# Kernel tuning notes

Measured on AMD Instinct MI355X. Metric: run time of the kernel, lower is better.

## Reference

```python
import jax, jax.numpy as jnp
import numpy as np
import math

B, S, D, H, L, V = 2, 2048, 1024, 16, 2, 32000
HD = D // H          # head_dim = 64
FF = 4 * D           # ffn hidden = 4096
NEG_INF = -1e9


def setup_inputs() -> dict:
    key = jax.random.key(0)
    ks = jax.random.split(key, 12)
    w = lambda k, shape: jax.random.normal(k, shape, dtype=jnp.float32) * 0.02
    return {
        "tokens": jax.random.randint(ks[0], (B, S), 0, V),
        "tok_emb": w(ks[1], (V, D)),
        "pos_emb": w(ks[2], (S, D)),
        # torch nn.Linear weights are [out, in]; stacked over layers
        "wq": w(ks[3], (L, D, D)),
        "wk": w(ks[4], (L, D, D)),
        "wv": w(ks[5], (L, D, D)),
        "wo": w(ks[6], (L, D, D)),
        "w1": w(ks[7], (L, FF, D)),
        "w2": w(ks[8], (L, D, FF)),
        "ln1_g": jnp.ones((L, D)), "ln1_b": jnp.zeros((L, D)),
        "ln2_g": jnp.ones((L, D)), "ln2_b": jnp.zeros((L, D)),
        "lnf_g": jnp.ones((D,)), "lnf_b": jnp.zeros((D,)),
        "w_out": w(ks[9], (V, D)),
    }


def _layernorm(x, g, b):
    m = jnp.mean(x, axis=-1, keepdims=True)
    v = jnp.mean(jnp.square(x - m), axis=-1, keepdims=True)
    return (x - m) * jax.lax.rsqrt(v + 1e-5) * g + b


def _transformer(tokens, tok_emb, pos_emb, wq, wk, wv, wo, w1, w2,
                 ln1_g, ln1_b, ln2_g, ln2_b, lnf_g, lnf_b, w_out):
    s = tokens.shape[1]
    # causal additive mask [1,1,S,S]
    mask = jnp.where(jnp.tril(jnp.ones((s, s), dtype=bool)), 0.0, NEG_INF)[None, None]
    h = tok_emb[tokens] + pos_emb[None, :s]
    scale = 1.0 / math.sqrt(HD)
    for l in range(L):
        # pre-norm attention
        a_in = _layernorm(h, ln1_g[l], ln1_b[l])
        q = (a_in @ wq[l].T).reshape(B, s, H, HD)
        k = (a_in @ wk[l].T).reshape(B, s, H, HD)
        v = (a_in @ wv[l].T).reshape(B, s, H, HD)
        scores = jnp.einsum('bqhd,bkhd->bhqk', q, k) * scale + mask
        attn = jax.nn.softmax(scores.astype(jnp.float32), axis=-1).astype(h.dtype)
        o = jnp.einsum('bhqk,bkhd->bqhd', attn, v).reshape(B, s, D)
        h = h + o @ wo[l].T
        # pre-norm ReLU FFN
        f_in = _layernorm(h, ln2_g[l], ln2_b[l])
        h = h + jax.nn.relu(f_in @ w1[l].T) @ w2[l].T
    h = _layernorm(h, lnf_g, lnf_b)
    return h @ w_out.T  # [B,S,V]


def reference(tokens, tok_emb, pos_emb, wq, wk, wv, wo, w1, w2,
              ln1_g, ln1_b, ln2_g, ln2_b, lnf_g, lnf_b, w_out):
    return _transformer(tokens, tok_emb, pos_emb, wq, wk, wv, wo, w1, w2,
                        ln1_g, ln1_b, ln2_g, ln2_b, lnf_g, lnf_b, w_out)
```

## Files before the change

### kernel.cpp

```cpp
#include <hip/hip_runtime.h>

#define Bv 2
#define Sv 2048
#define Dv 1024
#define Hv 16
#define HDv 64
#define FFv 4096
#define Vv 32000

typedef short bf16x8 __attribute__((ext_vector_type(8)));
typedef float f32x4 __attribute__((ext_vector_type(4)));
typedef unsigned short us8 __attribute__((ext_vector_type(8)));
typedef unsigned short us4 __attribute__((ext_vector_type(4)));
typedef unsigned short u16;

__device__ __forceinline__ u16 f2bf(float f) {
  union { float f; unsigned u; } x; x.f = f;
  x.u += 0x7fffu + ((x.u >> 16) & 1u);
  return (u16)(x.u >> 16);
}
__device__ __forceinline__ u16 f2bf_rtz(float f) {
  union { float f; unsigned u; } x; x.f = f;
  return (u16)(x.u >> 16);
}

__device__ __forceinline__ void gld16(const void* g, void* l) {
  __builtin_amdgcn_global_load_lds(
      (const __attribute__((address_space(1))) unsigned*)g,
      (__attribute__((address_space(3))) unsigned*)l, 16, 0, 0);
}

__global__ __launch_bounds__(256) void k_embed(const int* __restrict__ tok,
    const float* __restrict__ te, const float* __restrict__ pe,
    float* __restrict__ h) {
  int row = blockIdx.x;
  int s = row & (Sv - 1);
  int t = tok[row];
  float4 va = ((const float4*)(te + (size_t)t * Dv))[threadIdx.x];
  float4 vb = ((const float4*)(pe + (size_t)s * Dv))[threadIdx.x];
  float4 o;
  o.x = va.x + vb.x; o.y = va.y + vb.y; o.z = va.z + vb.z; o.w = va.w + vb.w;
  ((float4*)(h + (size_t)row * Dv))[threadIdx.x] = o;
}

__global__ __launch_bounds__(256) void k_cvt(const float* __restrict__ x,
    u16* __restrict__ y, int n4) {
  int i = blockIdx.x * 256 + threadIdx.x;
  if (i >= n4) return;
  float4 v = ((const float4*)x)[i];
  us4 o = { f2bf(v.x), f2bf(v.y), f2bf(v.z), f2bf(v.w) };
  ((us4*)y)[i] = o;
}

__global__ __launch_bounds__(256) void k_ln(const float* __restrict__ x,
    const float* __restrict__ g, const float* __restrict__ bb,
    u16* __restrict__ y) {
  int row = blockIdx.x, t = threadIdx.x;
  float4 v = ((const float4*)(x + (size_t)row * Dv))[t];
  float s = v.x + v.y + v.z + v.w;
#pragma unroll
  for (int m = 32; m; m >>= 1) s += __shfl_xor(s, m, 64);
  __shared__ float red[4];
  if ((t & 63) == 0) red[t >> 6] = s;
  __syncthreads();
  float mean = (red[0] + red[1] + red[2] + red[3]) * (1.0f / Dv);
  __syncthreads();
  float dx = v.x - mean, dy = v.y - mean, dz = v.z - mean, dw = v.w - mean;
  float s2 = dx * dx + dy * dy + dz * dz + dw * dw;
#pragma unroll
  for (int m = 32; m; m >>= 1) s2 += __shfl_xor(s2, m, 64);
  if ((t & 63) == 0) red[t >> 6] = s2;
  __syncthreads();
  float var = (red[0] + red[1] + red[2] + red[3]) * (1.0f / Dv);
  float rstd = rsqrtf(var + 1e-5f);
  float4 gg = ((const float4*)g)[t];
  float4 be = ((const float4*)bb)[t];
  us4 o = { f2bf(dx * rstd * gg.x + be.x), f2bf(dy * rstd * gg.y + be.y),
            f2bf(dz * rstd * gg.z + be.z), f2bf(dw * rstd * gg.w + be.w) };
  ((us4*)(y + (size_t)row * Dv))[t] = o;
}

__device__ __forceinline__ void stage32(const u16* __restrict__ g, int ldK,
    u16* lds, int row_base, int kt, int lane) {
  int row = row_base + (lane >> 2);
  int slot = (lane & 3) ^ ((row >> 1) & 3);
  const u16* src = g + (size_t)row * ldK + (kt << 5) + (slot << 3);
  gld16(src, lds + (row_base << 5));
}
__device__ __forceinline__ bf16x8 ldfragA(const u16* lds, int row, int ks) {
  return *(const bf16x8*)((const char*)lds + row * 64 + ((ks ^ ((row >> 1) & 3)) << 4));
}

template <int EPI>
__global__ __launch_bounds__(512, 4) void k_gemm8(const u16* __restrict__ A,
    const u16* __restrict__ Bm, const float* __restrict__ res,
    float* __restrict__ Cf, u16* __restrict__ Cb, int M, int N, int K) {
  __shared__ u16 As[2][128 * 32];
  __shared__ u16 Bs[2][256 * 32];
  int TM = M >> 7, TN = N >> 8, nwg = TM * TN;
  int orig = blockIdx.x;
  int qd = nwg >> 3, rm = nwg & 7, xcd = orig & 7;
  int wg = (xcd < rm ? xcd * (qd + 1) : rm * (qd + 1) + (xcd - rm) * qd) + (orig >> 3);
  int bm = wg % TM, bn = wg / TM;
  int m0 = bm << 7, n0 = bn << 8;
  int lane = threadIdx.x & 63, wid = threadIdx.x >> 6;
  int wr = wid >> 2, wc = wid & 3;
  int NT = K >> 5;
  const u16* Ag = A + (size_t)m0 * K;
  const u16* Bg = Bm + (size_t)n0 * K;
  int frow = lane & 15, ks = lane >> 4;

  f32x4 acc[4][4] = {};
  bf16x8 af[4], bf[4];

#pragma unroll
  for (int tt = 0; tt < 2; tt++) {
    stage32(Ag, K, As[tt], wid * 16, tt, lane);
    stage32(Bg, K, Bs[tt], wid * 32, tt, lane);
    stage32(Bg, K, Bs[tt], wid * 32 + 16, tt, lane);
  }
  asm volatile("s_waitcnt vmcnt(3)" ::: "memory");
  __builtin_amdgcn_s_barrier();

  for (int t = 0; t < NT; t++) {
    int p = t & 1;
    const u16* Ab = As[p];
    const u16* Bb = Bs[p];
#pragma unroll
    for (int f = 0; f < 4; f++) af[f] = ldfragA(Ab, wr * 64 + f * 16 + frow, ks);
#pragma unroll
    for (int n = 0; n < 4; n++) bf[n] = ldfragA(Bb, wc * 64 + n * 16 + frow, ks);
    asm volatile("s_waitcnt lgkmcnt(0)" ::: "memory");
    __builtin_amdgcn_sched_barrier(0);
    __builtin_amdgcn_s_barrier();
    if (t + 2 < NT) {
      stage32(Ag, K, As[p], wid * 16, t + 2, lane);
      stage32(Bg, K, Bs[p], wid * 32, t + 2, lane);
      stage32(Bg, K, Bs[p], wid * 32 + 16, t + 2, lane);
    }
    __builtin_amdgcn_s_setprio(1);
#pragma unroll
    for (int f = 0; f < 4; f++)
#pragma unroll
      for (int n = 0; n < 4; n++)
        acc[f][n] = __builtin_amdgcn_mfma_f32_16x16x32_bf16(af[f], bf[n], acc[f][n], 0, 0, 0);
    __builtin_amdgcn_s_setprio(0);
    __builtin_amdgcn_sched_barrier(0);
    if (t + 2 < NT) { asm volatile("s_waitcnt vmcnt(3)" ::: "memory"); }
    else            { asm volatile("s_waitcnt vmcnt(0)" ::: "memory"); }
    __builtin_amdgcn_s_barrier();
  }

#pragma unroll
  for (int f = 0; f < 4; f++) {
#pragma unroll
    for (int r = 0; r < 4; r++) {
      int row = m0 + wr * 64 + f * 16 + (lane >> 4) * 4 + r;
#pragma unroll
      for (int n = 0; n < 4; n++) {
        int col = n0 + wc * 64 + n * 16 + frow;
        float val = acc[f][n][r];
        size_t idx = (size_t)row * N + col;
        if constexpr (EPI == 1) { Cf[idx] = val + res[idx]; }
        else if constexpr (EPI == 0) { __builtin_nontemporal_store(val, &Cf[idx]); }
        else if constexpr (EPI == 2) { Cb[idx] = f2bf(val); }
        else { Cb[idx] = f2bf(fmaxf(val, 0.0f)); }
      }
    }
  }
}

template <int EPI>
__global__ __launch_bounds__(256, 4) void k_gemmn(const u16* __restrict__ A,
    const u16* __restrict__ Bm, const float* __restrict__ res,
    float* __restrict__ Cf, u16* __restrict__ Cb, int M, int N, int K) {
  __shared__ u16 As[2][64 * 32];
  __shared__ u16 Bs[2][128 * 32];
  int TM = M >> 6, TN = N >> 7, nwg = TM * TN;
  int orig = blockIdx.x;
  int qd = nwg >> 3, rm = nwg & 7, xcd = orig & 7;
  int wg = (xcd < rm ? xcd * (qd + 1) : rm * (qd + 1) + (xcd - rm) * qd) + (orig >> 3);
  int bm = wg % TM, bn = wg / TM;
  int m0 = bm << 6, n0 = bn << 7;
  int lane = threadIdx.x & 63, wid = threadIdx.x >> 6;
  int wr = wid >> 1, wc = wid & 1;
  int NT = K >> 5;
  const u16* Ag = A + (size_t)m0 * K;
  const u16* Bg = Bm + (size_t)n0 * K;
  int frow = lane & 15, ks = lane >> 4;

  f32x4 acc[2][4] = {};
  bf16x8 af[2], bf[4];

#pragma unroll
  for (int tt = 0; tt < 2; tt++) {
    stage32(Ag, K, As[tt], wid * 16, tt, lane);
    stage32(Bg, K, Bs[tt], wid * 32, tt, lane);
    stage32(Bg, K, Bs[tt], wid * 32 + 16, tt, lane);
  }
  asm volatile("s_waitcnt vmcnt(3)" ::: "memory");
  __builtin_amdgcn_s_barrier();

  for (int t = 0; t < NT; t++) {
    int p = t & 1;
    const u16* Ab = As[p];
    const u16* Bb = Bs[p];
#pragma unroll
    for (int f = 0; f < 2; f++) af[f] = ldfragA(Ab, wr * 32 + f * 16 + frow, ks);
#pragma unroll
    for (int n = 0; n < 4; n++) bf[n] = ldfragA(Bb, wc * 64 + n * 16 + frow, ks);
    asm volatile("s_waitcnt lgkmcnt(0)" ::: "memory");
    __builtin_amdgcn_sched_barrier(0);
    __builtin_amdgcn_s_barrier();
    if (t + 2 < NT) {
      stage32(Ag, K, As[p], wid * 16, t + 2, lane);
      stage32(Bg, K, Bs[p], wid * 32, t + 2, lane);
      stage32(Bg, K, Bs[p], wid * 32 + 16, t + 2, lane);
    }
    __builtin_amdgcn_s_setprio(1);
#pragma unroll
    for (int f = 0; f < 2; f++)
#pragma unroll
      for (int n = 0; n < 4; n++)
        acc[f][n] = __builtin_amdgcn_mfma_f32_16x16x32_bf16(af[f], bf[n], acc[f][n], 0, 0, 0);
    __builtin_amdgcn_s_setprio(0);
    __builtin_amdgcn_sched_barrier(0);
    if (t + 2 < NT) { asm volatile("s_waitcnt vmcnt(3)" ::: "memory"); }
    else            { asm volatile("s_waitcnt vmcnt(0)" ::: "memory"); }
    __builtin_amdgcn_s_barrier();
  }

#pragma unroll
  for (int f = 0; f < 2; f++) {
#pragma unroll
    for (int r = 0; r < 4; r++) {
      int row = m0 + wr * 32 + f * 16 + (lane >> 4) * 4 + r;
#pragma unroll
      for (int n = 0; n < 4; n++) {
        int col = n0 + wc * 64 + n * 16 + frow;
        float val = acc[f][n][r];
        size_t idx = (size_t)row * N + col;
        if constexpr (EPI == 1) { Cf[idx] = val + res[idx]; }
        else if constexpr (EPI == 0) { __builtin_nontemporal_store(val, &Cf[idx]); }
        else if constexpr (EPI == 2) { Cb[idx] = f2bf(val); }
        else { Cb[idx] = f2bf(fmaxf(val, 0.0f)); }
      }
    }
  }
}

__global__ __launch_bounds__(256) void k_transpose(const u16* __restrict__ v,
    u16* __restrict__ vt, int stride) {
  int st = blockIdx.x & 31;
  int bh = blockIdx.x >> 5;
  int b = bh >> 4, hh = bh & 15;
  __shared__ u16 tile[64][72];
  int t = threadIdx.x;
  int rr = t >> 3, cc = (t & 7) << 3;
#pragma unroll
  for (int it = 0; it < 2; it++) {
    int r = rr + it * 32;
    us8 val = *(const us8*)(v + (size_t)(b * Sv + st * 64 + r) * stride + hh * HDv + cc);
    *(us8*)&tile[r][cc] = val;
  }
  __syncthreads();
#pragma unroll
  for (int it = 0; it < 2; it++) {
    int d = rr + it * 32;
    us8 val;
#pragma unroll
    for (int j = 0; j < 8; j++) val[j] = tile[cc + j][d];
    *(us8*)(vt + ((size_t)bh * HDv + d) * Sv + st * 64 + cc) = val;
  }
}

__global__ __launch_bounds__(256) void k_attn(const u16* __restrict__ qg,
    const u16* __restrict__ kg, const u16* __restrict__ vt,
    u16* __restrict__ og) {
  int qt = blockIdx.x & 15;
  int bh = blockIdx.x >> 4;
  int b = bh >> 4, hh = bh & 15;
  int wv = threadIdx.x >> 6, lane = threadIdx.x & 63;
  int q0 = qt * 128 + wv * 32;
  __shared__ u16 plds_s[4][32 * 40];
  u16* plds = plds_s[wv];
  const int QS = 3 * Dv;
  const float sc2 = 0.18033688f;
  int qcol = lane & 15, g = lane >> 4;

  bf16x8 onesf;
#pragma unroll
  for (int j = 0; j < 8; j++) onesf[j] = (short)0x3F80;

  bf16x8 qf[2][2];
#pragma unroll
  for (int fm = 0; fm < 2; fm++)
#pragma unroll
    for (int dh = 0; dh < 2; dh++)
      qf[fm][dh] = *(const bf16x8*)(qg + (size_t)(b * Sv + q0 + fm * 16 + qcol) * QS
                                    + hh * HDv + dh * 32 + g * 8);

  f32x4 oacc[2][4] = {};
  f32x4 sacc[2] = {};

  int ktmax = (q0 + 31) >> 5;
  for (int kt = 0; kt <= ktmax; kt++) {
    int k0 = kt * 32;
    bf16x8 kf[2][2];
#pragma unroll
    for (int kn = 0; kn < 2; kn++)
#pragma unroll
      for (int dh = 0; dh < 2; dh++)
        kf[kn][dh] = *(const bf16x8*)(kg + (size_t)(b * Sv + k0 + kn * 16 + qcol) * QS
                                      + hh * HDv + dh * 32 + g * 8);
    f32x4 sa[2][2] = {};
#pragma unroll
    for (int dh = 0; dh < 2; dh++)
#pragma unroll
      for (int fm = 0; fm < 2; fm++)
#pragma unroll
        for (int kn = 0; kn < 2; kn++)
          sa[fm][kn] = __builtin_amdgcn_mfma_f32_16x16x32_bf16(kf[kn][dh], qf[fm][dh], sa[fm][kn], 0, 0, 0);

    bool full = (k0 + 31 <= q0);
#pragma unroll
    for (int fm = 0; fm < 2; fm++) {
      int qrow = q0 + fm * 16 + qcol;
      float pv[2][4];
#pragma unroll
      for (int kn = 0; kn < 2; kn++)
#pragma unroll
        for (int r = 0; r < 4; r++) {
          float e = exp2f(sa[fm][kn][r] * sc2);
          if (!full && (k0 + kn * 16 + g * 4 + r) > qrow) e = 0.0f;
          pv[kn][r] = e;
        }
#pragma unroll
      for (int kn = 0; kn < 2; kn++) {
        us4 pk = { f2bf_rtz(pv[kn][0]), f2bf_rtz(pv[kn][1]),
                   f2bf_rtz(pv[kn][2]), f2bf_rtz(pv[kn][3]) };
        *(us4*)(plds + (fm * 16 + qcol) * 40 + kn * 16 + g * 4) = pk;
      }
    }
    bf16x8 pf[2];
#pragma unroll
    for (int fm = 0; fm < 2; fm++)
      pf[fm] = *(const bf16x8*)(plds + (fm * 16 + qcol) * 40 + g * 8);
    bf16x8 vf[4];
#pragma unroll
    for (int dn = 0; dn < 4; dn++)
      vf[dn] = *(const bf16x8*)(vt + ((size_t)bh * HDv + dn * 16 + qcol) * Sv
                                + k0 + g * 8);
#pragma unroll
    for (int fm = 0; fm < 2; fm++) {
      sacc[fm] = __builtin_amdgcn_mfma_f32_16x16x32_bf16(pf[fm], onesf, sacc[fm], 0, 0, 0);
#pragma unroll
      for (int dn = 0; dn < 4; dn++)
        oacc[fm][dn] = __builtin_amdgcn_mfma_f32_16x16x32_bf16(pf[fm], vf[dn], oacc[fm][dn], 0, 0, 0);
    }
  }

#pragma unroll
  for (int fm = 0; fm < 2; fm++)
#pragma unroll
    for (int r = 0; r < 4; r++) {
      float li = 1.0f / sacc[fm][r];
      int row = q0 + fm * 16 + g * 4 + r;
#pragma unroll
      for (int dn = 0; dn < 4; dn++)
        og[(size_t)(b * Sv + row) * Dv + hh * HDv + dn * 16 + qcol] =
            f2bf(oacc[fm][dn][r] * li);
    }
}

extern "C" void kernel_launch(void* const* d_in, const int* in_sizes, int n_in,
                              void* d_out, int out_size, void* d_ws, size_t ws_size,
                              hipStream_t stream) {
  const int*   tok  = (const int*)d_in[0];
  const float* te   = (const float*)d_in[1];
  const float* pe   = (const float*)d_in[2];
  const float* wq   = (const float*)d_in[3];
  const float* wk   = (const float*)d_in[4];
  const float* wvv  = (const float*)d_in[5];
  const float* wo   = (const float*)d_in[6];
  const float* w1   = (const float*)d_in[7];
  const float* w2   = (const float*)d_in[8];
  const float* ln1g = (const float*)d_in[9];
  const float* ln1b = (const float*)d_in[10];
  const float* ln2g = (const float*)d_in[11];
  const float* ln2b = (const float*)d_in[12];
  const float* lnfg = (const float*)d_in[13];
  const float* lnfb = (const float*)d_in[14];
  const float* wout = (const float*)d_in[15];
  float* out = (float*)d_out;

  char* p = (char*)d_ws;
  float* h  = (float*)p; p += (size_t)4096 * 1024 * 4;
  u16* a    = (u16*)p;   p += (size_t)4096 * 1024 * 2;
  u16* qkv  = (u16*)p;   p += (size_t)4096 * 3072 * 2;
  u16* vt   = (u16*)p;   p += (size_t)32 * 64 * 2048 * 2;
  u16* o    = (u16*)p;   p += (size_t)4096 * 1024 * 2;
  u16* f1   = (u16*)p;   p += (size_t)4096 * 4096 * 2;
  u16* wb   = (u16*)p;   p += (size_t)32000 * 1024 * 2;

  const int M = Bv * Sv;

  k_embed<<<M, 256, 0, stream>>>(tok, te, pe, h);
  for (int l = 0; l < 2; l++) {
    k_ln<<<M, 256, 0, stream>>>(h, ln1g + l * Dv, ln1b + l * Dv, a);
    k_cvt<<<1024, 256, 0, stream>>>(wq  + (size_t)l * Dv * Dv, wb,              (Dv * Dv) / 4);
    k_cvt<<<1024, 256, 0, stream>>>(wk  + (size_t)l * Dv * Dv, wb + Dv * Dv,    (Dv * Dv) / 4);
    k_cvt<<<1024, 256, 0, stream>>>(wvv + (size_t)l * Dv * Dv, wb + 2 * Dv * Dv,(Dv * Dv) / 4);
    k_gemm8<2><<<32 * 12, 512, 0, stream>>>(a, wb, nullptr, nullptr, qkv, M, 3 * Dv, Dv);
    k_transpose<<<1024, 256, 0, stream>>>(qkv + 2 * Dv, vt, 3 * Dv);
    k_attn<<<512, 256, 0, stream>>>(qkv, qkv + Dv, vt, o);
    k_cvt<<<1024, 256, 0, stream>>>(wo + (size_t)l * Dv * Dv, wb, (Dv * Dv) / 4);
    k_gemmn<1><<<64 * 8, 256, 0, stream>>>(o, wb, h, h, nullptr, M, Dv, Dv);
    k_ln<<<M, 256, 0, stream>>>(h, ln2g + l * Dv, ln2b + l * Dv, a);
    k_cvt<<<4096, 256, 0, stream>>>(w1 + (size_t)l * FFv * Dv, wb, (FFv * Dv) / 4);
    k_gemm8<3><<<32 * 16, 512, 0, stream>>>(a, wb, nullptr, nullptr, f1, M, FFv, Dv);
    k_cvt<<<4096, 256, 0, stream>>>(w2 + (size_t)l * Dv * FFv, wb, (Dv * FFv) / 4);
    k_gemmn<1><<<64 * 8, 256, 0, stream>>>(f1, wb, h, h, nullptr, M, Dv, FFv);
  }
  k_ln<<<M, 256, 0, stream>>>(h, lnfg, lnfb, a);
  k_cvt<<<32000, 256, 0, stream>>>(wout, wb, (Vv * Dv) / 4);
  k_gemm8<0><<<32 * 125, 512, 0, stream>>>(a, wb, nullptr, out, nullptr, M, Vv, Dv);
}
```

Before: 956.7 us.

## Triple-buffer GEMM LDS stages and split attention into heavy-first single-wave blocks

```diff
diff --git a/kernel.cpp b/kernel.cpp
--- a/kernel.cpp
+++ b/kernel.cpp
@@ -95,8 +95,8 @@
 __global__ __launch_bounds__(512, 4) void k_gemm8(const u16* __restrict__ A,
     const u16* __restrict__ Bm, const float* __restrict__ res,
     float* __restrict__ Cf, u16* __restrict__ Cb, int M, int N, int K) {
-  __shared__ u16 As[2][128 * 32];
-  __shared__ u16 Bs[2][256 * 32];
+  __shared__ u16 As[3][128 * 32];
+  __shared__ u16 Bs[3][256 * 32];
   int TM = M >> 7, TN = N >> 8, nwg = TM * TN;
   int orig = blockIdx.x;
   int qd = nwg >> 3, rm = nwg & 7, xcd = orig & 7;
@@ -122,8 +122,14 @@
   asm volatile("s_waitcnt vmcnt(3)" ::: "memory");
   __builtin_amdgcn_s_barrier();
 
+  int p = 0;
   for (int t = 0; t < NT; t++) {
-    int p = t & 1;
+    int q = p + 2 >= 3 ? p - 1 : p + 2;
+    if (t + 2 < NT) {
+      stage32(Ag, K, As[q], wid * 16, t + 2, lane);
+      stage32(Bg, K, Bs[q], wid * 32, t + 2, lane);
+      stage32(Bg, K, Bs[q], wid * 32 + 16, t + 2, lane);
+    }
     const u16* Ab = As[p];
     const u16* Bb = Bs[p];
 #pragma unroll
@@ -132,12 +138,6 @@
     for (int n = 0; n < 4; n++) bf[n] = ldfragA(Bb, wc * 64 + n * 16 + frow, ks);
     asm volatile("s_waitcnt lgkmcnt(0)" ::: "memory");
     __builtin_amdgcn_sched_barrier(0);
-    __builtin_amdgcn_s_barrier();
-    if (t + 2 < NT) {
-      stage32(Ag, K, As[p], wid * 16, t + 2, lane);
-      stage32(Bg, K, Bs[p], wid * 32, t + 2, lane);
-      stage32(Bg, K, Bs[p], wid * 32 + 16, t + 2, lane);
-    }
     __builtin_amdgcn_s_setprio(1);
 #pragma unroll
     for (int f = 0; f < 4; f++)
@@ -149,6 +149,7 @@
     if (t + 2 < NT) { asm volatile("s_waitcnt vmcnt(3)" ::: "memory"); }
     else            { asm volatile("s_waitcnt vmcnt(0)" ::: "memory"); }
     __builtin_amdgcn_s_barrier();
+    p = p + 1 >= 3 ? 0 : p + 1;
   }
 
 #pragma unroll
@@ -174,8 +175,8 @@
 __global__ __launch_bounds__(256, 4) void k_gemmn(const u16* __restrict__ A,
     const u16* __restrict__ Bm, const float* __restrict__ res,
     float* __restrict__ Cf, u16* __restrict__ Cb, int M, int N, int K) {
-  __shared__ u16 As[2][64 * 32];
-  __shared__ u16 Bs[2][128 * 32];
+  __shared__ u16 As[3][64 * 32];
+  __shared__ u16 Bs[3][128 * 32];
   int TM = M >> 6, TN = N >> 7, nwg = TM * TN;
   int orig = blockIdx.x;
   int qd = nwg >> 3, rm = nwg & 7, xcd = orig & 7;
@@ -201,8 +202,14 @@
   asm volatile("s_waitcnt vmcnt(3)" ::: "memory");
   __builtin_amdgcn_s_barrier();
 
+  int p = 0;
   for (int t = 0; t < NT; t++) {
-    int p = t & 1;
+    int q = p + 2 >= 3 ? p - 1 : p + 2;
+    if (t + 2 < NT) {
+      stage32(Ag, K, As[q], wid * 16, t + 2, lane);
+      stage32(Bg, K, Bs[q], wid * 32, t + 2, lane);
+      stage32(Bg, K, Bs[q], wid * 32 + 16, t + 2, lane);
+    }
     const u16* Ab = As[p];
     const u16* Bb = Bs[p];
 #pragma unroll
@@ -211,12 +218,6 @@
     for (int n = 0; n < 4; n++) bf[n] = ldfragA(Bb, wc * 64 + n * 16 + frow, ks);
     asm volatile("s_waitcnt lgkmcnt(0)" ::: "memory");
     __builtin_amdgcn_sched_barrier(0);
-    __builtin_amdgcn_s_barrier();
-    if (t + 2 < NT) {
-      stage32(Ag, K, As[p], wid * 16, t + 2, lane);
-      stage32(Bg, K, Bs[p], wid * 32, t + 2, lane);
-      stage32(Bg, K, Bs[p], wid * 32 + 16, t + 2, lane);
-    }
     __builtin_amdgcn_s_setprio(1);
 #pragma unroll
     for (int f = 0; f < 2; f++)
@@ -228,6 +229,7 @@
     if (t + 2 < NT) { asm volatile("s_waitcnt vmcnt(3)" ::: "memory"); }
     else            { asm volatile("s_waitcnt vmcnt(0)" ::: "memory"); }
     __builtin_amdgcn_s_barrier();
+    p = p + 1 >= 3 ? 0 : p + 1;
   }
 
 #pragma unroll
@@ -274,16 +276,17 @@
   }
 }
 
-__global__ __launch_bounds__(256) void k_attn(const u16* __restrict__ qg,
+__global__ __launch_bounds__(64) void k_attn(const u16* __restrict__ qg,
     const u16* __restrict__ kg, const u16* __restrict__ vt,
     u16* __restrict__ og) {
-  int qt = blockIdx.x & 15;
-  int bh = blockIdx.x >> 4;
+  int bid = blockIdx.x;
+  int qt = 15 - (bid >> 7);
+  int bh = (bid >> 2) & 31;
+  int strip = bid & 3;
   int b = bh >> 4, hh = bh & 15;
-  int wv = threadIdx.x >> 6, lane = threadIdx.x & 63;
-  int q0 = qt * 128 + wv * 32;
-  __shared__ u16 plds_s[4][32 * 40];
-  u16* plds = plds_s[wv];
+  int lane = threadIdx.x;
+  int q0 = qt * 128 + strip * 32;
+  __shared__ u16 plds[32 * 40];
   const int QS = 3 * Dv;
   const float sc2 = 0.18033688f;
   int qcol = lane & 15, g = lane >> 4;
@@ -302,10 +305,11 @@
 
   f32x4 oacc[2][4] = {};
   f32x4 sacc[2] = {};
-
-  int ktmax = (q0 + 31) >> 5;
-  for (int kt = 0; kt <= ktmax; kt++) {
+  int nfull = q0 >> 5;
+
+  for (int kt = 0; kt <= nfull; kt++) {
     int k0 = kt * 32;
+    bool diag = (kt == nfull);
     bf16x8 kf[2][2];
 #pragma unroll
     for (int kn = 0; kn < 2; kn++)
@@ -322,17 +326,16 @@
         for (int kn = 0; kn < 2; kn++)
           sa[fm][kn] = __builtin_amdgcn_mfma_f32_16x16x32_bf16(kf[kn][dh], qf[fm][dh], sa[fm][kn], 0, 0, 0);
 
-    bool full = (k0 + 31 <= q0);
 #pragma unroll
     for (int fm = 0; fm < 2; fm++) {
-      int qrow = q0 + fm * 16 + qcol;
+      int qrow = fm * 16 + qcol;
       float pv[2][4];
 #pragma unroll
       for (int kn = 0; kn < 2; kn++)
 #pragma unroll
         for (int r = 0; r < 4; r++) {
           float e = exp2f(sa[fm][kn][r] * sc2);
-          if (!full && (k0 + kn * 16 + g * 4 + r) > qrow) e = 0.0f;
+          if (diag && (kn * 16 + g * 4 + r) > qrow) e = 0.0f;
           pv[kn][r] = e;
         }
 #pragma unroll
@@ -413,7 +416,7 @@
     k_cvt<<<1024, 256, 0, stream>>>(wvv + (size_t)l * Dv * Dv, wb + 2 * Dv * Dv,(Dv * Dv) / 4);
     k_gemm8<2><<<32 * 12, 512, 0, stream>>>(a, wb, nullptr, nullptr, qkv, M, 3 * Dv, Dv);
     k_transpose<<<1024, 256, 0, stream>>>(qkv + 2 * Dv, vt, 3 * Dv);
-    k_attn<<<512, 256, 0, stream>>>(qkv, qkv + Dv, vt, o);
+    k_attn<<<2048, 64, 0, stream>>>(qkv, qkv + Dv, vt, o);
     k_cvt<<<1024, 256, 0, stream>>>(wo + (size_t)l * Dv * Dv, wb, (Dv * Dv) / 4);
     k_gemmn<1><<<64 * 8, 256, 0, stream>>>(o, wb, h, h, nullptr, M, Dv, Dv);
     k_ln<<<M, 256, 0, stream>>>(h, ln2g + l * Dv, ln2b + l * Dv, a);
```

New measurement: 933.3 us. -2.4%, faster.
